# Kernel optimization log

Measured on AMD Instinct MI355X. Metric: run time of the kernel, lower is better.

The kernel has to match this reference:

```python
import jax, jax.numpy as jnp
import numpy as np

K = 1024   # in_dim = out_dim = per-head dim (module uses full k per head)
H = 4      # heads
B, T = 2, 2048


def setup_inputs() -> dict:
    key = jax.random.key(0)
    ks = jax.random.split(key, 7)
    s = 0.02
    return {
        "x": jax.random.normal(ks[0], (B, T, K), jnp.float32),
        "Wq": jax.random.normal(ks[1], (K, K * H), jnp.float32) * s,
        "Wk": jax.random.normal(ks[2], (K, K * H), jnp.float32) * s,
        "Wv": jax.random.normal(ks[3], (K, K * H), jnp.float32) * s,
        "Wu": jax.random.normal(ks[4], (K * H, K), jnp.float32) * s,
        "bu": jnp.zeros((K,), jnp.float32),
        "W1": jax.random.normal(ks[5], (K, K), jnp.float32) * s,
        "b1": jnp.zeros((K,), jnp.float32),
        "W2": jax.random.normal(ks[6], (K, K), jnp.float32) * s,
        "b2": jnp.zeros((K,), jnp.float32),
    }


def reference(x, Wq, Wk, Wv, Wu, bu, W1, b1, W2, b2):
    b, t, k = x.shape
    h = H
    scale = k ** (-0.25)
    # projections: each head gets FULL dim k (quirk of the original module)
    q = (x @ Wq).reshape(b, t, h, k) * scale   # [b,t,h,k]
    kk = (x @ Wk).reshape(b, t, h, k) * scale
    v = (x @ Wv).reshape(b, t, h, k)
    # attention scores [b,h,q,k_pos]
    dot = jnp.einsum("bqhd,bkhd->bhqk", q, kk)
    causal = jnp.tril(jnp.ones((t, t), bool))  # strictly-upper masked to -inf
    dot = jnp.where(causal, dot, -jnp.inf)
    attn = jax.nn.softmax(dot, axis=-1)
    out = jnp.einsum("bhqk,bkhd->bqhd", attn, v).reshape(b, t, h * k)
    attn_out = out @ Wu + bu                   # unifyheads
    x = x + attn_out                            # residual
    ff = jax.nn.relu(x @ W1 + b1) @ W2 + b2     # in_dim == out_dim
    return x + ff                               # residual around FFN
```

## Files before the change

### kernel.cpp

```cpp
#include <hip/hip_runtime.h>
#include <math.h>


typedef __attribute__((ext_vector_type(8))) short short8;
typedef __attribute__((ext_vector_type(4))) float f32x4;

__device__ __forceinline__ unsigned short f2bf(float f) {
  union { float f; unsigned int u; } v; v.f = f;
  unsigned int r = (v.u + 0x7fffu + ((v.u >> 16) & 1u)) >> 16;
  return (unsigned short)r;
}
__device__ __forceinline__ float bf2f(unsigned short b) {
  union { unsigned int u; float f; } v; v.u = ((unsigned int)b) << 16;
  return v.f;
}

#define GL2LDS(g, l)                                                          \
  __builtin_amdgcn_global_load_lds(                                           \
      (__attribute__((address_space(1))) void*)(g),                           \
      (__attribute__((address_space(3))) void*)(l), 16, 0, 0)

__device__ __forceinline__ void core256(
    const unsigned short* __restrict__ A, const unsigned short* __restrict__ BT,
    int m0, int n0, int kmax, int lda, int ldb, int ldc, long long coff,
    unsigned short* __restrict__ Cb, unsigned short* lds) {
  const int tid = threadIdx.x;
  const int lane = tid & 63;
  const int wid = tid >> 6;
  const int wm = wid >> 2;
  const int wn = wid & 3;

  unsigned short* Als = lds;
  unsigned short* Bls = lds + 32768;

  const int srow = wid * 8 + (lane >> 3);
  const int scol = ((lane & 7) ^ (lane >> 3)) * 8;
  const unsigned short* ag = A + (long long)(m0 + srow) * lda + scol;
  const unsigned short* bg = BT + (long long)(n0 + srow) * ldb + scol;

  const int frow = lane & 15;
  const int lq = lane >> 4;
  const int fsw = frow & 7;

  f32x4 acc[8][4];
#pragma unroll
  for (int i = 0; i < 8; ++i)
#pragma unroll
    for (int j = 0; j < 4; ++j) acc[i][j] = {0.f, 0.f, 0.f, 0.f};

  short8 afr[4][2];
  short8 bfrE[2][2];
  short8 bfrO[2][2];

  const int NT = kmax >> 6;

  auto stageA = [&](int t_, int h_) {
    unsigned short* d = Als + (t_ & 1) * 16384 + h_ * 8192 + wid * 512;
    const unsigned short* g = ag + ((long long)h_ * 128) * lda + t_ * 64;
    GL2LDS(g, d);
    GL2LDS(g + (long long)64 * lda, d + 4096);
  };
  auto stageB = [&](int t_, int h_) {
    unsigned short* d = Bls + (t_ & 1) * 16384 + h_ * 8192 + wid * 512;
    const unsigned short* g = bg + ((long long)h_ * 128) * ldb + t_ * 64;
    GL2LDS(g, d);
    GL2LDS(g + (long long)64 * ldb, d + 4096);
  };

#define RDA(BUF, QM)                                                          \
  _Pragma("unroll")                                                           \
  for (int m_ = 0; m_ < 4; ++m_)                                              \
    _Pragma("unroll")                                                         \
    for (int kh_ = 0; kh_ < 2; ++kh_)                                         \
      afr[m_][kh_] = *(const short8*)(Als + (BUF) * 16384 + wm * 8192 +       \
          ((QM) * 64 + m_ * 16 + frow) * 64 + ((kh_ * 4 + lq) ^ fsw) * 8);

#define RDB(BUF, QN, BFR)                                                     \
  _Pragma("unroll")                                                           \
  for (int n_ = 0; n_ < 2; ++n_)                                              \
    _Pragma("unroll")                                                         \
    for (int kh_ = 0; kh_ < 2; ++kh_)                                         \
      BFR[n_][kh_] = *(const short8*)(Bls + (BUF) * 16384 + (wn >> 1) * 8192 +\
          ((wn & 1) * 64 + (QN) * 32 + n_ * 16 + frow) * 64 +                 \
          ((kh_ * 4 + lq) ^ fsw) * 8);

#define QUAD(QM, QN, BFR)                                                     \
  do {                                                                        \
    __builtin_amdgcn_s_setprio(1);                                            \
    _Pragma("unroll")                                                         \
    for (int m_ = 0; m_ < 4; ++m_)                                            \
      _Pragma("unroll")                                                       \
      for (int n_ = 0; n_ < 2; ++n_)                                          \
        _Pragma("unroll")                                                     \
        for (int kh_ = 0; kh_ < 2; ++kh_)                                     \
          acc[(QM) * 4 + m_][(QN) * 2 + n_] =                                 \
              __builtin_amdgcn_mfma_f32_16x16x32_bf16(                        \
                  afr[m_][kh_], BFR[n_][kh_],                                 \
                  acc[(QM) * 4 + m_][(QN) * 2 + n_], 0, 0, 0);                \
    __builtin_amdgcn_s_setprio(0);                                            \
  } while (0)

  stageA(0, 0); stageA(0, 1); stageB(0, 0); stageB(0, 1);
  asm volatile("s_waitcnt vmcnt(0)" ::: "memory");
  __builtin_amdgcn_s_barrier();
  RDA(0, 0)
  RDB(0, 0, bfrE)

  for (int t = 0; t < NT; ++t) {
    const int b = t & 1;
    const bool pf = (t + 1 < NT);
    if (pf) { stageA(t + 1, 0); stageA(t + 1, 1); }
    QUAD(0, 0, bfrE);
    RDB(b, 1, bfrO)
    if (pf) { stageB(t + 1, 0); stageB(t + 1, 1); }
    QUAD(0, 1, bfrO);
    RDA(b, 1)
    QUAD(1, 0, bfrE);
    QUAD(1, 1, bfrO);
    asm volatile("s_waitcnt vmcnt(0)" ::: "memory");
    __builtin_amdgcn_s_barrier();
    if (pf) {
      RDA(b ^ 1, 0)
      RDB(b ^ 1, 0, bfrE)
    }
  }
#undef RDA
#undef RDB
#undef QUAD

  const int ccol = lane & 15;
  const int crow = lq * 4;
#pragma unroll
  for (int mi = 0; mi < 8; ++mi) {
#pragma unroll
    for (int ni = 0; ni < 4; ++ni) {
      const int gc = n0 + wn * 64 + ni * 16 + ccol;
#pragma unroll
      for (int r = 0; r < 4; ++r) {
        const int gr = m0 + wm * 128 + mi * 16 + crow + r;
        Cb[coff + (long long)gr * ldc + gc] = f2bf(acc[mi][ni][r]);
      }
    }
  }
}


__global__ __launch_bounds__(512, 2) void g256_cmb(
    const unsigned short* __restrict__ Wkc,
    const unsigned short* __restrict__ Wqc,
    unsigned short* __restrict__ Wcomb) {
  __shared__ unsigned short lds[65536];
  const long long Mi = 1024 * 1024;
  const int bid = blockIdx.x;
  const int z = bid & 7, zb = z >> 2, zh = z & 3;
  const int j = bid >> 3;
  const int m0 = (j & 3) * 256, n0 = (j >> 2) * 256;
  core256(Wkc + (long long)zb * 4 * Mi + zh * 1024,
          Wqc + (long long)zb * 4 * Mi + zh * 1024,
          m0, n0, 1024, 4096, 4096, 1024,
          (long long)zb * 4 * Mi + (long long)zh * Mi, Wcomb, lds);
}

__global__ __launch_bounds__(512, 2) void g256_t(
    const unsigned short* __restrict__ xb,
    const unsigned short* __restrict__ Wcomb,
    unsigned short* __restrict__ tb) {
  __shared__ unsigned short lds[65536];
  const int bid = blockIdx.x;
  const int xcd = bid & 7;
  const int j = bid >> 3;
  const int m0 = (xcd * 2 + (j & 1)) * 256;
  const int n0 = (j >> 1) * 256;
  core256(xb, Wcomb, m0, n0, 1024, 1024, 1024, 4096, 0, tb, lds);
}

__global__ __launch_bounds__(512, 2) void g256_sv(
    const unsigned short* __restrict__ xb,
    const unsigned short* __restrict__ Wcomb,
    const unsigned short* __restrict__ tb,
    unsigned short* __restrict__ S, unsigned short* __restrict__ vT) {
  __shared__ unsigned short lds[65536];
  const long long TT = (long long)2048 * 2048;
  const int bid = blockIdx.x;
  if (bid < 288) {
    const int z = bid & 7, zb = z >> 2, zh = z & 3;
    const int idx = bid >> 3;
    int m = (int)((sqrtf(8.0f * idx + 1.0f) - 1.0f) * 0.5f);
    while ((m + 1) * (m + 2) / 2 <= idx) ++m;
    while (m * (m + 1) / 2 > idx) --m;
    const int m0 = m * 256;
    const int n0 = (idx - m * (m + 1) / 2) * 256;
    core256(tb + (long long)zb * 2048 * 4096 + zh * 1024,
            xb + (long long)zb * 2048 * 1024,
            m0, n0, 1024, 4096, 1024, 2048,
            (long long)(zb * 4 + zh) * TT, S, lds);
  } else {
    const int r = bid - 288;
    const int xcd = r & 7;
    const int j = r >> 3;
    const int m0 = (xcd * 2 + (j & 1)) * 256;
    const int rest = j >> 1;
    const int bb = rest >> 3;
    const int n0 = (rest & 7) * 256;
    core256(Wcomb + (size_t)4096 * 1024, xb + (long long)bb * 2048 * 1024,
            m0, n0, 1024, 1024, 1024, 2048, (long long)bb * 4096 * 2048,
            vT, lds);
  }
}

__global__ __launch_bounds__(512, 2) void g256_pv(
    const unsigned short* __restrict__ S, const unsigned short* __restrict__ vT,
    unsigned short* __restrict__ Pb) {
  __shared__ unsigned short lds[65536];
  const long long TT = (long long)2048 * 2048;
  const long long MN = (long long)4096 * 1024;
  const int z = blockIdx.x, zb = z >> 2, zh = z & 3;
  const int m0 = blockIdx.y * 256, n0 = blockIdx.z * 256;
  core256(S + (long long)(zb * 4 + zh) * TT,
          vT + (long long)zb * 4096 * 2048 + (long long)zh * 1024 * 2048,
          m0, n0, m0 + 256, 2048, 2048, 1024,
          (long long)zh * MN + (long long)zb * 2048 * 1024, Pb, lds);
}

__device__ __forceinline__ void core64(
    f32x4 acc[4][2], const unsigned short* __restrict__ A, int lda,
    const unsigned short* __restrict__ BT, int ldb, int kmax,
    unsigned short* As, unsigned short* Bs) {
  const int tid = threadIdx.x;
  const int lane = tid & 63;
  const int wv = tid >> 6;
  const int wm = wv & 1;
  const int wn = wv >> 1;
  const int srow = tid >> 2;
  const int scol = (((tid & 3) ^ ((srow >> 1) & 3)) * 8);
  const unsigned short* ap0 = A + (long long)srow * lda + scol;
  const unsigned short* ap1 = ap0 + (long long)64 * lda;
  const unsigned short* bp0 = BT + (long long)srow * ldb + scol;
  unsigned short* lA = As + wv * 512;
  unsigned short* lB = Bs + wv * 512;
  const int frow = lane & 15;
  const int fqs = (((lane >> 4) ^ ((frow >> 1) & 3)) * 8);

  int rs = 0, rc = 0;

  auto stage = [&]() {
    unsigned short* a = lA + rs * 4096;
    GL2LDS(ap0, a); GL2LDS(ap1, a + 2048);
    GL2LDS(bp0, lB + rs * 2048);
    ap0 += 32; ap1 += 32; bp0 += 32;
    rs ^= 1;
  };
  auto compute = [&]() {
    const unsigned short* Ac = As + rc * 4096;
    const unsigned short* Bc = Bs + rc * 2048;
    short8 afr[4], bfr[2];
#pragma unroll
    for (int mi = 0; mi < 4; ++mi)
      afr[mi] = *(const short8*)(Ac + (wm * 64 + mi * 16 + frow) * 32 + fqs);
#pragma unroll
    for (int ni = 0; ni < 2; ++ni)
      bfr[ni] = *(const short8*)(Bc + (wn * 32 + ni * 16 + frow) * 32 + fqs);
    __builtin_amdgcn_s_setprio(1);
#pragma unroll
    for (int mi = 0; mi < 4; ++mi)
#pragma unroll
      for (int ni = 0; ni < 2; ++ni)
        acc[mi][ni] = __builtin_amdgcn_mfma_f32_16x16x32_bf16(
            afr[mi], bfr[ni], acc[mi][ni], 0, 0, 0);
    __builtin_amdgcn_s_setprio(0);
    rc ^= 1;
  };

  const int nsteps = kmax >> 5;
  stage();
  for (int i = 0; i + 1 < nsteps; ++i) {
    stage();
    asm volatile("s_waitcnt vmcnt(3)" ::: "memory");
    __builtin_amdgcn_s_barrier();
    __builtin_amdgcn_sched_barrier(0);
    compute();
    __builtin_amdgcn_sched_barrier(0);
    __builtin_amdgcn_s_barrier();
  }
  asm volatile("s_waitcnt vmcnt(0)" ::: "memory");
  __builtin_amdgcn_s_barrier();
  __builtin_amdgcn_sched_barrier(0);
  compute();
}

__global__ __launch_bounds__(256) void gemm_ffn(
    const unsigned short* __restrict__ A, const unsigned short* __restrict__ BT,
    const float* __restrict__ bias, const float* __restrict__ resid,
    int do_relu, float* __restrict__ Cf, unsigned short* __restrict__ Cb) {
  __shared__ unsigned short As[8192];
  __shared__ unsigned short Bs[4096];
  const int bid = blockIdx.x;
  const int xcd = bid & 7;
  const int j = bid >> 3;
  const int m0 = (xcd * 4 + (j & 3)) * 128;
  const int n0 = (j >> 2) * 64;
  f32x4 acc[4][2];
#pragma unroll
  for (int i = 0; i < 4; ++i)
#pragma unroll
    for (int j2 = 0; j2 < 2; ++j2) acc[i][j2] = {0.f, 0.f, 0.f, 0.f};
  core64(acc, A + (long long)m0 * 1024, 1024, BT + (long long)n0 * 1024, 1024,
         1024, As, Bs);
  const int lane = threadIdx.x & 63;
  const int wv = threadIdx.x >> 6;
  const int wm = wv & 1, wn = wv >> 1;
  const int ccol = lane & 15, crow = (lane >> 4) * 4;
#pragma unroll
  for (int mi = 0; mi < 4; ++mi) {
#pragma unroll
    for (int ni = 0; ni < 2; ++ni) {
      const int gc = n0 + wn * 32 + ni * 16 + ccol;
#pragma unroll
      for (int r = 0; r < 4; ++r) {
        const int gr = m0 + wm * 64 + mi * 16 + crow + r;
        float v = acc[mi][ni][r] + bias[gc];
        if (resid) v += resid[(long long)gr * 1024 + gc];
        if (do_relu) v = fmaxf(v, 0.f);
        const long long ci = (long long)gr * 1024 + gc;
        if (Cf) Cf[ci] = v;
        if (Cb) Cb[ci] = f2bf(v);
      }
    }
  }
}

__global__ __launch_bounds__(256) void reduce_epi(
    const unsigned short* __restrict__ Pb, int S, long long MN,
    const float* __restrict__ bias, const float* __restrict__ resid,
    int do_relu, float* __restrict__ Cf, unsigned short* __restrict__ Cb) {
  const long long i4 = ((long long)blockIdx.x * 256 + threadIdx.x) * 4;
  if (i4 >= MN) return;
  float4 s = {0.f, 0.f, 0.f, 0.f};
  for (int t = 0; t < S; ++t) {
    const ushort4 p = *(const ushort4*)(Pb + (long long)t * MN + i4);
    s.x += bf2f(p.x); s.y += bf2f(p.y); s.z += bf2f(p.z); s.w += bf2f(p.w);
  }
  if (bias) {
    const int c0 = (int)(i4 & 1023);
    s.x += bias[c0]; s.y += bias[c0 + 1]; s.z += bias[c0 + 2]; s.w += bias[c0 + 3];
  }
  if (resid) {
    const float4 rr = *(const float4*)(resid + i4);
    s.x += rr.x; s.y += rr.y; s.z += rr.z; s.w += rr.w;
  }
  if (do_relu) {
    s.x = fmaxf(s.x, 0.f); s.y = fmaxf(s.y, 0.f);
    s.z = fmaxf(s.z, 0.f); s.w = fmaxf(s.w, 0.f);
  }
  if (Cf) *(float4*)(Cf + i4) = s;
  if (Cb) {
    ushort4 o;
    o.x = f2bf(s.x); o.y = f2bf(s.y); o.z = f2bf(s.z); o.w = f2bf(s.w);
    *(ushort4*)(Cb + i4) = o;
  }
}

__global__ __launch_bounds__(256) void softmax_causal(unsigned short* S, int T) {
  const int q = blockIdx.x;
  unsigned short* row = S + ((long long)blockIdx.y * T + q) * T;
  const int tid = threadIdx.x;
  const int lane = tid & 63;
  const int wv = tid >> 6;
  const int n = q + 1;
  const int nz = (n + 255) & ~255;
  const int base = tid * 8;
  short8 raw = {};
  if (base < nz) raw = *(const short8*)(row + base);
  float vals[8];
  float m = -__builtin_inff();
#pragma unroll
  for (int i = 0; i < 8; ++i) {
    vals[i] = (base + i < n) ? bf2f((unsigned short)raw[i]) : -__builtin_inff();
    m = fmaxf(m, vals[i]);
  }
#pragma unroll
  for (int o = 32; o; o >>= 1) m = fmaxf(m, __shfl_xor(m, o, 64));
  __shared__ float red[4];
  if (lane == 0) red[wv] = m;
  __syncthreads();
  m = fmaxf(fmaxf(red[0], red[1]), fmaxf(red[2], red[3]));
  __syncthreads();
  float s = 0.f, e[8];
#pragma unroll
  for (int i = 0; i < 8; ++i) {
    e[i] = (base + i < n) ? __expf(vals[i] - m) : 0.f;
    s += e[i];
  }
#pragma unroll
  for (int o = 32; o; o >>= 1) s += __shfl_xor(s, o, 64);
  if (lane == 0) red[wv] = s;
  __syncthreads();
  s = red[0] + red[1] + red[2] + red[3];
  const float inv = 1.f / s;
  if (base < nz) {
    short8 o8;
#pragma unroll
    for (int i = 0; i < 8; ++i) o8[i] = (short)f2bf(e[i] * inv);
    *(short8*)(row + base) = o8;
  }
}

__global__ __launch_bounds__(256) void prep_all(
    const float* __restrict__ x, const float* __restrict__ Wq,
    const float* __restrict__ Wk, const float* __restrict__ Wv,
    const float* __restrict__ Wu, const float* __restrict__ W1,
    const float* __restrict__ W2, unsigned short* __restrict__ xb,
    unsigned short* __restrict__ Wqc, unsigned short* __restrict__ Wkc,
    unsigned short* __restrict__ Wvc, unsigned short* __restrict__ WuTb,
    unsigned short* __restrict__ W1T, unsigned short* __restrict__ W2T,
    float s2) {
  const int z = blockIdx.y;
  if (z <= 3) {
    const float* src = (z == 0) ? x : (z == 1) ? Wq : (z == 2) ? Wk : Wv;
    unsigned short* dst = (z == 0) ? xb : (z == 1) ? Wqc : (z == 2) ? Wkc : Wvc;
    const float sc = (z == 2) ? s2 : 1.0f;
    const long long i4 = ((long long)blockIdx.x * 256 + threadIdx.x) * 4;
    const float4 v = *(const float4*)(src + i4);
    ushort4 u;
    u.x = f2bf(v.x * sc); u.y = f2bf(v.y * sc);
    u.z = f2bf(v.z * sc); u.w = f2bf(v.w * sc);
    *(ushort4*)(dst + i4) = u;
    return;
  }
  const int R = (z == 4) ? 4096 : 1024;
  const int by = blockIdx.x >> 5;
  if (by * 32 >= R) return;
  const float* W = (z == 4) ? Wu : (z == 5) ? W1 : W2;
  unsigned short* WT = (z == 4) ? WuTb : (z == 5) ? W1T : W2T;
  __shared__ float tile[32][33];
  const int c0 = (blockIdx.x & 31) * 32;
  const int r0 = by * 32;
  const int tx = threadIdx.x & 31;
  const int ty = threadIdx.x >> 5;
#pragma unroll
  for (int j = 0; j < 32; j += 8)
    tile[ty + j][tx] = W[(long long)(r0 + ty + j) * 1024 + c0 + tx];
  __syncthreads();
#pragma unroll
  for (int j = 0; j < 32; j += 8)
    WT[(long long)(c0 + ty + j) * R + r0 + tx] = f2bf(tile[tx][ty + j]);
}

extern "C" void kernel_launch(void* const* d_in, const int* in_sizes, int n_in,
                              void* d_out, int out_size, void* d_ws,
                              size_t ws_size, hipStream_t stream) {
  (void)in_sizes; (void)n_in; (void)out_size; (void)ws_size;
  const float* x  = (const float*)d_in[0];
  const float* Wq = (const float*)d_in[1];
  const float* Wk = (const float*)d_in[2];
  const float* Wv = (const float*)d_in[3];
  const float* Wu = (const float*)d_in[4];
  const float* bu = (const float*)d_in[5];
  const float* W1 = (const float*)d_in[6];
  const float* b1 = (const float*)d_in[7];
  const float* W2 = (const float*)d_in[8];
  const float* b2 = (const float*)d_in[9];
  float* out = (float*)d_out;

  const int T = 2048;
  const size_t MB = 1024 * 1024;
  const long long MN = (long long)4096 * 1024;

  char* w = (char*)d_ws;
  unsigned short* xb    = (unsigned short*)(w + 0 * MB);
  unsigned short* Wqc   = (unsigned short*)(w + 8 * MB);
  unsigned short* Wvc   = (unsigned short*)(w + 16 * MB);
  unsigned short* Wkc   = (unsigned short*)(w + 24 * MB);
  unsigned short* WuTb  = (unsigned short*)(w + 32 * MB);
  unsigned short* Wcomb = (unsigned short*)(w + 40 * MB);
  unsigned short* tb    = (unsigned short*)(w + 56 * MB);
  unsigned short* vT    = (unsigned short*)(w + 88 * MB);
  unsigned short* S     = (unsigned short*)(w + 120 * MB);
  unsigned short* W1T   = (unsigned short*)(w + 184 * MB);
  unsigned short* W2T   = (unsigned short*)(w + 186 * MB);
  unsigned short* Pb    = (unsigned short*)(w + 40 * MB);
  float*          x1f   = (float*)(w + 8 * MB);
  unsigned short* x1b   = (unsigned short*)(w + 24 * MB);
  unsigned short* h1    = (unsigned short*)(w + 32 * MB);
  (void)WuTb; (void)Wvc;

  const float s2 = 0.03125f;

  prep_all<<<dim3(4096, 7), 256, 0, stream>>>(
      x, Wq, Wk, Wv, Wu, W1, W2, xb, Wqc, Wkc, Wvc, WuTb, W1T, W2T, s2);

  g256_cmb<<<dim3(128), 512, 0, stream>>>(Wkc, Wqc, Wcomb);

  g256_t<<<dim3(256), 512, 0, stream>>>(xb, Wcomb, tb);

  g256_sv<<<dim3(544), 512, 0, stream>>>(xb, Wcomb, tb, S, vT);

  softmax_causal<<<dim3(T, 8), 256, 0, stream>>>(S, T);

  g256_pv<<<dim3(8, 8, 4), 512, 0, stream>>>(S, vT, Pb);

  reduce_epi<<<dim3(4096), 256, 0, stream>>>(Pb, 4, MN, bu, x, 0, x1f, x1b);

  gemm_ffn<<<dim3(512), 256, 0, stream>>>(x1b, W1T, b1, nullptr, 1,
                                          nullptr, h1);

  gemm_ffn<<<dim3(512), 256, 0, stream>>>(h1, W2T, b2, x1f, 0, out, nullptr);
}
```

Baseline: 403.8 us.

## Stagger quadrant order between wave parities and unroll main loop by two

Odd and even waves now walk the four MFMA quadrants in opposite order, so their LDS fragment reads and MFMA bursts are out of phase and contend less for LDS bandwidth. The K loop is unrolled by two so the double-buffer indices become compile-time constants. The unrolled loop assumes NT is even; an odd NT would skip the last tile. Code size and register pressure also rise.

```diff
diff --git a/kernel.cpp b/kernel.cpp
--- a/kernel.cpp
+++ b/kernel.cpp
@@ -29,6 +29,7 @@
   const int wid = tid >> 6;
   const int wm = wid >> 2;
   const int wn = wid & 3;
+  const int par = __builtin_amdgcn_readfirstlane(wid & 1);
 
   unsigned short* Als = lds;
   unsigned short* Bls = lds + 32768;
@@ -103,25 +104,58 @@
   stageA(0, 0); stageA(0, 1); stageB(0, 0); stageB(0, 1);
   asm volatile("s_waitcnt vmcnt(0)" ::: "memory");
   __builtin_amdgcn_s_barrier();
-  RDA(0, 0)
-  RDB(0, 0, bfrE)
-
-  for (int t = 0; t < NT; ++t) {
-    const int b = t & 1;
-    const bool pf = (t + 1 < NT);
-    if (pf) { stageA(t + 1, 0); stageA(t + 1, 1); }
-    QUAD(0, 0, bfrE);
-    RDB(b, 1, bfrO)
-    if (pf) { stageB(t + 1, 0); stageB(t + 1, 1); }
-    QUAD(0, 1, bfrO);
-    RDA(b, 1)
-    QUAD(1, 0, bfrE);
-    QUAD(1, 1, bfrO);
+  if (par == 0) { RDA(0, 0) RDB(0, 0, bfrE) }
+  else          { RDA(0, 1) RDB(0, 1, bfrO) }
+
+  const int NTP = NT >> 1;
+  for (int i = 0; i < NTP; ++i) {
+    const int t0 = i * 2;
+    const bool pf2 = (i + 1 < NTP);
+    stageA(t0 + 1, 0); stageA(t0 + 1, 1);
+    if (par == 0) {
+      QUAD(0, 0, bfrE);
+      RDB(0, 1, bfrO)
+      stageB(t0 + 1, 0); stageB(t0 + 1, 1);
+      QUAD(0, 1, bfrO);
+      RDA(0, 1)
+      QUAD(1, 0, bfrE);
+      QUAD(1, 1, bfrO);
+    } else {
+      QUAD(1, 1, bfrO);
+      RDB(0, 0, bfrE)
+      stageB(t0 + 1, 0); stageB(t0 + 1, 1);
+      QUAD(1, 0, bfrE);
+      RDA(0, 0)
+      QUAD(0, 1, bfrO);
+      QUAD(0, 0, bfrE);
+    }
     asm volatile("s_waitcnt vmcnt(0)" ::: "memory");
     __builtin_amdgcn_s_barrier();
-    if (pf) {
-      RDA(b ^ 1, 0)
-      RDB(b ^ 1, 0, bfrE)
+    if (par == 0) { RDA(1, 0) RDB(1, 0, bfrE) }
+    else          { RDA(1, 1) RDB(1, 1, bfrO) }
+    if (pf2) { stageA(t0 + 2, 0); stageA(t0 + 2, 1); }
+    if (par == 0) {
+      QUAD(0, 0, bfrE);
+      RDB(1, 1, bfrO)
+      if (pf2) { stageB(t0 + 2, 0); stageB(t0 + 2, 1); }
+      QUAD(0, 1, bfrO);
+      RDA(1, 1)
+      QUAD(1, 0, bfrE);
+      QUAD(1, 1, bfrO);
+    } else {
+      QUAD(1, 1, bfrO);
+      RDB(1, 0, bfrE)
+      if (pf2) { stageB(t0 + 2, 0); stageB(t0 + 2, 1); }
+      QUAD(1, 0, bfrE);
+      RDA(1, 0)
+      QUAD(0, 1, bfrO);
+      QUAD(0, 0, bfrE);
+    }
+    asm volatile("s_waitcnt vmcnt(0)" ::: "memory");
+    __builtin_amdgcn_s_barrier();
+    if (pf2) {
+      if (par == 0) { RDA(0, 0) RDB(0, 0, bfrE) }
+      else          { RDA(0, 1) RDB(0, 1, bfrO) }
     }
   }
 #undef RDA
```

Result: slower. 1.459 ms (+261.4%).
